# Optimization experiments

Measured on AMD Instinct MI355X. Metric: run time of the kernel, lower is better.

Reference implementation:

```python
import jax, jax.numpy as jnp
import numpy as np

N = 100000
E = 1600000
IN_C, HID_C, OUT_C = 128, 64, 32


def _add_self_loops(edge_index, n):
    loops = jnp.arange(n, dtype=edge_index.dtype)
    src = jnp.concatenate([edge_index[0], loops])
    dst = jnp.concatenate([edge_index[1], loops])
    return src, dst


def _gcn_norm(src, dst, n):
    # symmetric normalization on A + I with unit edge weights
    deg = jax.ops.segment_sum(jnp.ones_like(dst, dtype=jnp.float32), dst, num_segments=n)
    dinv = jnp.where(deg > 0, jax.lax.rsqrt(deg), 0.0)
    return dinv[src] * dinv[dst]  # [E+N]


def _gcn_conv(x, src, dst, norm, W, b, n):
    h = x @ W                              # [N, out]
    msg = h[src] * norm[:, None]           # [E+N, out]  (dominant gather)
    out = jax.ops.segment_sum(msg, dst, num_segments=n)
    return out + b


def setup_inputs() -> dict:
    key = jax.random.key(0)
    k = jax.random.split(key, 6)
    x = jax.random.normal(k[0], (N, IN_C), dtype=jnp.float32)
    edge_index = jax.random.randint(k[1], (2, E), 0, N, dtype=jnp.int32)
    # Glorot-style init for GCN weights
    W1 = jax.random.normal(k[2], (IN_C, HID_C), dtype=jnp.float32) / np.sqrt(IN_C)
    b1 = jnp.zeros((HID_C,), dtype=jnp.float32)
    W2 = jax.random.normal(k[3], (HID_C, OUT_C), dtype=jnp.float32) / np.sqrt(HID_C)
    b2 = jnp.zeros((OUT_C,), dtype=jnp.float32)
    return {"x": x, "edge_index": edge_index, "W1": W1, "b1": b1, "W2": W2, "b2": b2}


def reference(x, edge_index, W1, b1, W2, b2):
    src, dst = _add_self_loops(edge_index, N)
    norm = _gcn_norm(src, dst, N)
    h = _gcn_conv(x, src, dst, norm, W1, b1, N)
    h = jax.nn.relu(h)
    # dropout p=0.2 is identity in eval mode
    out = _gcn_conv(h, src, dst, norm, W2, b2, N)
    return out
```

## Files before the change

kernel.cpp:

```cpp
#include <hip/hip_runtime.h>
#include <hip/hip_fp16.h>

#define N_NODES 100000
#define E_EDGES 1600000
#define IN_C 128
#define HID_C 64
#define OUT_C 32
#define BNODES 64
#define NBUCK ((N_NODES + BNODES - 1) / BNODES)
#define MAXB 2048
#define NCHUNK 256
#define CHUNK_E (E_EDGES / NCHUNK)

__device__ __forceinline__ int chunk_of_block(int b) { return (b & 7) * (NCHUNK / 8) + (b >> 3); }

__global__ void zero_gcur_kernel(int* __restrict__ gcur) {
    int i = blockIdx.x * 256 + threadIdx.x;
    if (i < NBUCK) gcur[i] = 0;
}

__global__ __launch_bounds__(1024) void bucket_scatter_kernel(const int* __restrict__ src,
                                                              const int* __restrict__ dst,
                                                              int* __restrict__ gcur,
                                                              unsigned* __restrict__ pairs) {
    __shared__ int h[NBUCK];
    for (int i = threadIdx.x; i < NBUCK; i += 1024) h[i] = 0;
    __syncthreads();
    const int chunk = chunk_of_block(blockIdx.x);
    const int base = chunk * CHUNK_E;
    int dc[7];
    int nj = 0;
    for (int j = threadIdx.x; j < CHUNK_E; j += 1024) {
        int d = dst[base + j];
        dc[nj++] = d;
        atomicAdd(&h[d >> 6], 1);
    }
    __syncthreads();
    for (int i = threadIdx.x; i < NBUCK; i += 1024) {
        int c = h[i];
        if (c > 0) h[i] = atomicAdd(&gcur[i], c);
    }
    __syncthreads();
    nj = 0;
    for (int j = threadIdx.x; j < CHUNK_E; j += 1024) {
        int d = dc[nj++];
        int pos = atomicAdd(&h[d >> 6], 1);
        pairs[(unsigned)(d >> 6) * MAXB + (unsigned)pos] =
            ((unsigned)src[base + j] << 6) | (unsigned)(d & 63);
    }
}

__global__ __launch_bounds__(256) void bucket_sort_kernel(const int* __restrict__ gcur,
                                                          unsigned* __restrict__ pairs,
                                                          int* __restrict__ row_beg,
                                                          int* __restrict__ row_end,
                                                          float* __restrict__ dinv) {
    __shared__ unsigned sp[MAXB];
    __shared__ int hcnt[BNODES], scn[BNODES], cur[BNODES];
    const int b = blockIdx.x;
    const int beg = b * MAXB;
    int cnt = gcur[b];
    if (cnt > MAXB) cnt = MAXB;
    if (threadIdx.x < BNODES) hcnt[threadIdx.x] = 0;
    __syncthreads();
    for (int j = threadIdx.x; j < cnt; j += 256) {
        unsigned p = pairs[beg + j];
        sp[j] = p;
        atomicAdd(&hcnt[p & 63], 1);
    }
    __syncthreads();
    if (threadIdx.x < BNODES) scn[threadIdx.x] = hcnt[threadIdx.x];
    __syncthreads();
    for (int off = 1; off < BNODES; off <<= 1) {
        int t = 0;
        if (threadIdx.x < BNODES && threadIdx.x >= off) t = scn[threadIdx.x - off];
        __syncthreads();
        if (threadIdx.x < BNODES) scn[threadIdx.x] += t;
        __syncthreads();
    }
    if (threadIdx.x < BNODES) {
        int ex = scn[threadIdx.x] - hcnt[threadIdx.x];
        cur[threadIdx.x] = ex;
        int node = b * BNODES + threadIdx.x;
        if (node < N_NODES) {
            row_beg[node] = beg + ex;
            row_end[node] = beg + ex + hcnt[threadIdx.x];
            dinv[node] = rsqrtf((float)hcnt[threadIdx.x] + 1.0f);
        }
    }
    __syncthreads();
    for (int j = threadIdx.x; j < cnt; j += 256) {
        unsigned p = sp[j];
        int pos = atomicAdd(&cur[p & 63], 1);
        pairs[beg + pos] = p >> 6;
    }
}

__global__ __launch_bounds__(256) void gemm1_kernel(const float* __restrict__ x,
                                                    const float* __restrict__ W1,
                                                    const float* __restrict__ dinv,
                                                    __half* __restrict__ hs) {
    __shared__ float sW[IN_C * HID_C];
    for (int i = threadIdx.x; i < IN_C * HID_C; i += 256) sW[i] = W1[i];
    __syncthreads();
    const int cg = (threadIdx.x & 7) * 8;
    const int row0 = blockIdx.x * 64 + (threadIdx.x >> 3) * 2;
    float acc[2][8];
#pragma unroll
    for (int r = 0; r < 2; ++r)
#pragma unroll
        for (int c = 0; c < 8; ++c) acc[r][c] = 0.f;

    int rr[2];
#pragma unroll
    for (int r = 0; r < 2; ++r) rr[r] = min(row0 + r, N_NODES - 1);

    const float4* x4 = (const float4*)x;
#pragma unroll 2
    for (int k4 = 0; k4 < IN_C / 4; ++k4) {
        float4 xv[2];
#pragma unroll
        for (int r = 0; r < 2; ++r) xv[r] = x4[(size_t)rr[r] * (IN_C / 4) + k4];
        float xs[2][4];
#pragma unroll
        for (int r = 0; r < 2; ++r) {
            xs[r][0] = xv[r].x; xs[r][1] = xv[r].y; xs[r][2] = xv[r].z; xs[r][3] = xv[r].w;
        }
#pragma unroll
        for (int kk = 0; kk < 4; ++kk) {
            const float4* wp = (const float4*)(sW + (k4 * 4 + kk) * HID_C + cg);
            float4 w0 = wp[0], w1 = wp[1];
            float wv[8] = {w0.x, w0.y, w0.z, w0.w, w1.x, w1.y, w1.z, w1.w};
#pragma unroll
            for (int r = 0; r < 2; ++r)
#pragma unroll
                for (int c = 0; c < 8; ++c)
                    acc[r][c] = fmaf(xs[r][kk], wv[c], acc[r][c]);
        }
    }
#pragma unroll
    for (int r = 0; r < 2; ++r) {
        int row = row0 + r;
        if (row < N_NODES) {
            float dv = dinv[row];
            union { float4 f; __half2 h[4]; } u;
#pragma unroll
            for (int q = 0; q < 4; ++q)
                u.h[q] = __floats2half2_rn(acc[r][2 * q] * dv, acc[r][2 * q + 1] * dv);
            *(float4*)(hs + (size_t)row * HID_C + cg) = u.f;
        }
    }
}

__global__ __launch_bounds__(256) void agg1_kernel(const int* __restrict__ row_beg,
                                                   const int* __restrict__ row_end,
                                                   const int* __restrict__ col,
                                                   const float2* __restrict__ hsf,
                                                   const float* __restrict__ dinv,
                                                   const float* __restrict__ b1,
                                                   const float* __restrict__ W2,
                                                   __half* __restrict__ gs) {
    __shared__ float sW[HID_C * OUT_C];
    __shared__ __half2 sh2[16][HID_C / 2];
    for (int i = threadIdx.x; i < HID_C * OUT_C; i += 256) sW[i] = W2[i];

    const int nl = threadIdx.x >> 4;
    const int node = blockIdx.x * 16 + nl;
    const int lane = threadIdx.x & 15;
    const int beg = row_beg[node], end = row_end[node];
    float2 u = hsf[(size_t)node * 16 + lane];
    __half2* uh = (__half2*)&u;
    float2 t0 = __half22float2(uh[0]), t1 = __half22float2(uh[1]);
    float a0 = t0.x, a1 = t0.y, a2 = t1.x, a3 = t1.y;

    int j = beg;
    int idx0 = j + (lane & 7);
    int cv = (idx0 < end) ? col[idx0] : 0;
    while (j + 8 <= end) {
        int jn = j + 8;
        int idxn = jn + (lane & 7);
        int cvn = (idxn < end) ? col[idxn] : 0;
        int s[8];
#pragma unroll
        for (int e = 0; e < 8; ++e) s[e] = __shfl(cv, e, 8);
        float2 v[8];
#pragma unroll
        for (int e = 0; e < 8; ++e) v[e] = hsf[(size_t)s[e] * 16 + lane];
        cv = cvn;
#pragma unroll
        for (int e = 0; e < 8; ++e) {
            __half2* vh = (__half2*)&v[e];
            float2 w0 = __half22float2(vh[0]), w1 = __half22float2(vh[1]);
            a0 += w0.x; a1 += w0.y; a2 += w1.x; a3 += w1.y;
        }
        j = jn;
    }
    const int tail = end - j;
    for (int e = 0; e < tail; ++e) {
        int s = __shfl(cv, e, 8);
        float2 v = hsf[(size_t)s * 16 + lane];
        __half2* vh = (__half2*)&v;
        float2 w0 = __half22float2(vh[0]), w1 = __half22float2(vh[1]);
        a0 += w0.x; a1 += w0.y; a2 += w1.x; a3 += w1.y;
    }
    const float dv = dinv[node];
    float4 bb = ((const float4*)b1)[lane];
    __half2 p0 = __floats2half2_rn(fmaxf(dv * a0 + bb.x, 0.f), fmaxf(dv * a1 + bb.y, 0.f));
    __half2 p1 = __floats2half2_rn(fmaxf(dv * a2 + bb.z, 0.f), fmaxf(dv * a3 + bb.w, 0.f));
    sh2[nl][lane * 2] = p0;
    sh2[nl][lane * 2 + 1] = p1;
    __syncthreads();

    const int oc = lane * 2;
    float o0 = 0.f, o1 = 0.f;
#pragma unroll
    for (int k2 = 0; k2 < HID_C / 2; ++k2) {
        float2 hv = __half22float2(sh2[nl][k2]);
        const float* w0 = sW + (2 * k2) * OUT_C + oc;
        const float* w1 = sW + (2 * k2 + 1) * OUT_C + oc;
        o0 = fmaf(hv.x, w0[0], o0); o1 = fmaf(hv.x, w0[1], o1);
        o0 = fmaf(hv.y, w1[0], o0); o1 = fmaf(hv.y, w1[1], o1);
    }
    *(__half2*)(gs + (size_t)node * OUT_C + oc) = __floats2half2_rn(o0 * dv, o1 * dv);
}

__global__ void agg2_kernel(const int* __restrict__ row_beg, const int* __restrict__ row_end,
                            const int* __restrict__ col,
                            const float2* __restrict__ gsf, const float* __restrict__ dinv,
                            const float* __restrict__ b2, float* __restrict__ out) {
    const int node = blockIdx.x * 32 + (threadIdx.x >> 3);
    const int lane = threadIdx.x & 7;
    if (node >= N_NODES) return;
    const int beg = row_beg[node], end = row_end[node];
    float2 u = gsf[(size_t)node * 8 + lane];
    __half2* uh = (__half2*)&u;
    float2 t0 = __half22float2(uh[0]), t1 = __half22float2(uh[1]);
    float a0 = t0.x, a1 = t0.y, a2 = t1.x, a3 = t1.y;

    int j = beg;
    int idx0 = j + lane;
    int cv = (idx0 < end) ? col[idx0] : 0;
    while (j + 8 <= end) {
        int jn = j + 8;
        int idxn = jn + lane;
        int cvn = (idxn < end) ? col[idxn] : 0;
        int s[8];
#pragma unroll
        for (int e = 0; e < 8; ++e) s[e] = __shfl(cv, e, 8);
        float2 v[8];
#pragma unroll
        for (int e = 0; e < 8; ++e) v[e] = gsf[(size_t)s[e] * 8 + lane];
        cv = cvn;
#pragma unroll
        for (int e = 0; e < 8; ++e) {
            __half2* vh = (__half2*)&v[e];
            float2 w0 = __half22float2(vh[0]), w1 = __half22float2(vh[1]);
            a0 += w0.x; a1 += w0.y; a2 += w1.x; a3 += w1.y;
        }
        j = jn;
    }
    const int tail = end - j;
    for (int e = 0; e < tail; ++e) {
        int s = __shfl(cv, e, 8);
        float2 v = gsf[(size_t)s * 8 + lane];
        __half2* vh = (__half2*)&v;
        float2 w0 = __half22float2(vh[0]), w1 = __half22float2(vh[1]);
        a0 += w0.x; a1 += w0.y; a2 += w1.x; a3 += w1.y;
    }
    float dv = dinv[node];
    float4 bb = ((const float4*)b2)[lane];
    float4 o;
    o.x = dv * a0 + bb.x;
    o.y = dv * a1 + bb.y;
    o.z = dv * a2 + bb.z;
    o.w = dv * a3 + bb.w;
    *(float4*)(out + (size_t)node * OUT_C + lane * 4) = o;
}

extern "C" void kernel_launch(void* const* d_in, const int* in_sizes, int n_in,
                              void* d_out, int out_size, void* d_ws, size_t ws_size,
                              hipStream_t stream) {
    const float* x  = (const float*)d_in[0];
    const int*   ei = (const int*)d_in[1];
    const float* W1 = (const float*)d_in[2];
    const float* b1 = (const float*)d_in[3];
    const float* W2 = (const float*)d_in[4];
    const float* b2 = (const float*)d_in[5];
    float* out = (float*)d_out;

    const int* srcv = ei;
    const int* dstv = ei + E_EDGES;

    float* dinv  = (float*)d_ws;
    __half* hs   = (__half*)(dinv + N_NODES);
    __half* gs   = hs + (size_t)N_NODES * HID_C;
    int* row_beg = (int*)(gs + (size_t)N_NODES * OUT_C);
    int* row_end = row_beg + N_NODES;
    int* gcur    = row_end + N_NODES;
    unsigned* pairs = (unsigned*)(gcur + 1568);
    int* col = (int*)pairs;

    zero_gcur_kernel<<<(NBUCK + 255) / 256, 256, 0, stream>>>(gcur);
    bucket_scatter_kernel<<<NCHUNK, 1024, 0, stream>>>(srcv, dstv, gcur, pairs);
    bucket_sort_kernel<<<NBUCK, 256, 0, stream>>>(gcur, pairs, row_beg, row_end, dinv);

    gemm1_kernel<<<(N_NODES + 63) / 64, 256, 0, stream>>>(x, W1, dinv, hs);

    agg1_kernel<<<N_NODES / 16, 256, 0, stream>>>(row_beg, row_end, col,
                                                  (const float2*)hs, dinv, b1, W2, gs);

    agg2_kernel<<<(N_NODES + 31) / 32, 256, 0, stream>>>(row_beg, row_end, col,
                                                         (const float2*)gs, dinv, b2, out);
}
```

Baseline: 126.8 us.

## Double-buffer neighbor gathers in aggregation kernels with prefetched tail chunk

Restructures both aggregation kernels so two 8-edge chunks of neighbor features are gathered ahead while the previous chunk is consumed, and the partial tail chunk is issued up front. More gathers are in flight per thread, which targets the latency of the random gathers. Index math also switches from 64-bit to 32-bit unsigned, and the shared-memory reads in the fused W2 projection are padded and vectorized. The cost is higher register pressure from three 8-element buffers, and the removed bounds check in agg2 assumes the grid exactly covers all nodes.

```diff
diff --git a/kernel.cpp b/kernel.cpp
--- a/kernel.cpp
+++ b/kernel.cpp
@@ -152,6 +152,20 @@
     }
 }
 
+#define AG_GATHER(V, CV, TBL, STRIDE)                                         \
+    _Pragma("unroll")                                                         \
+    for (int e = 0; e < 8; ++e) {                                             \
+        int s_ = __shfl((CV), e, 8);                                          \
+        (V)[e] = (TBL)[(unsigned)(s_ * (STRIDE) + lane)];                     \
+    }
+#define AG_CONSUME(V)                                                         \
+    _Pragma("unroll")                                                         \
+    for (int e = 0; e < 8; ++e) {                                             \
+        __half2* vh_ = (__half2*)&(V)[e];                                     \
+        float2 w0_ = __half22float2(vh_[0]), w1_ = __half22float2(vh_[1]);    \
+        a0 += w0_.x; a1 += w0_.y; a2 += w1_.x; a3 += w1_.y;                   \
+    }
+
 __global__ __launch_bounds__(256) void agg1_kernel(const int* __restrict__ row_beg,
                                                    const int* __restrict__ row_end,
                                                    const int* __restrict__ col,
@@ -161,48 +175,57 @@
                                                    const float* __restrict__ W2,
                                                    __half* __restrict__ gs) {
     __shared__ float sW[HID_C * OUT_C];
-    __shared__ __half2 sh2[16][HID_C / 2];
+    __shared__ __half2 sh2[16][HID_C / 2 + 1];
     for (int i = threadIdx.x; i < HID_C * OUT_C; i += 256) sW[i] = W2[i];
 
     const int nl = threadIdx.x >> 4;
     const int node = blockIdx.x * 16 + nl;
     const int lane = threadIdx.x & 15;
     const int beg = row_beg[node], end = row_end[node];
-    float2 u = hsf[(size_t)node * 16 + lane];
+    const int deg = end - beg;
+    const int F = deg >> 3;
+
+    float2 u = hsf[(unsigned)(node * 16 + lane)];
     __half2* uh = (__half2*)&u;
     float2 t0 = __half22float2(uh[0]), t1 = __half22float2(uh[1]);
     float a0 = t0.x, a1 = t0.y, a2 = t1.x, a3 = t1.y;
 
-    int j = beg;
-    int idx0 = j + (lane & 7);
-    int cv = (idx0 < end) ? col[idx0] : 0;
-    while (j + 8 <= end) {
-        int jn = j + 8;
-        int idxn = jn + (lane & 7);
-        int cvn = (idxn < end) ? col[idxn] : 0;
-        int s[8];
-#pragma unroll
-        for (int e = 0; e < 8; ++e) s[e] = __shfl(cv, e, 8);
-        float2 v[8];
-#pragma unroll
-        for (int e = 0; e < 8; ++e) v[e] = hsf[(size_t)s[e] * 16 + lane];
-        cv = cvn;
-#pragma unroll
-        for (int e = 0; e < 8; ++e) {
-            __half2* vh = (__half2*)&v[e];
+    float2 vA[8], vB[8], vT[8];
+    int cvA = 0, cvB = 0, cvT = 0;
+    if (F >= 1) { cvA = col[beg + (lane & 7)];     AG_GATHER(vA, cvA, hsf, 16); }
+    if (F >= 2) { cvB = col[beg + 8 + (lane & 7)]; AG_GATHER(vB, cvB, hsf, 16); }
+    {
+        int ti = beg + F * 8 + (lane & 7);
+        cvT = (ti < end) ? col[ti] : 0;
+        AG_GATHER(vT, cvT, hsf, 16);
+    }
+    int c = 0;
+    while (c + 2 < F) {
+        int cvN = col[beg + (c + 2) * 8 + (lane & 7)];
+        AG_CONSUME(vA);
+        AG_GATHER(vA, cvN, hsf, 16);
+        ++c;
+        if (c + 2 < F) {
+            int cvN2 = col[beg + (c + 2) * 8 + (lane & 7)];
+            AG_CONSUME(vB);
+            AG_GATHER(vB, cvN2, hsf, 16);
+            ++c;
+        }
+    }
+    while (c < F) {
+        if ((c & 1) == 0) { AG_CONSUME(vA); } else { AG_CONSUME(vB); }
+        ++c;
+    }
+    const int tail = deg & 7;
+#pragma unroll
+    for (int e = 0; e < 8; ++e) {
+        if (e < tail) {
+            __half2* vh = (__half2*)&vT[e];
             float2 w0 = __half22float2(vh[0]), w1 = __half22float2(vh[1]);
             a0 += w0.x; a1 += w0.y; a2 += w1.x; a3 += w1.y;
         }
-        j = jn;
-    }
-    const int tail = end - j;
-    for (int e = 0; e < tail; ++e) {
-        int s = __shfl(cv, e, 8);
-        float2 v = hsf[(size_t)s * 16 + lane];
-        __half2* vh = (__half2*)&v;
-        float2 w0 = __half22float2(vh[0]), w1 = __half22float2(vh[1]);
-        a0 += w0.x; a1 += w0.y; a2 += w1.x; a3 += w1.y;
-    }
+    }
+
     const float dv = dinv[node];
     float4 bb = ((const float4*)b1)[lane];
     __half2 p0 = __floats2half2_rn(fmaxf(dv * a0 + bb.x, 0.f), fmaxf(dv * a1 + bb.y, 0.f));
@@ -212,16 +235,17 @@
     __syncthreads();
 
     const int oc = lane * 2;
+    const float2* wp2 = (const float2*)sW;
     float o0 = 0.f, o1 = 0.f;
 #pragma unroll
     for (int k2 = 0; k2 < HID_C / 2; ++k2) {
         float2 hv = __half22float2(sh2[nl][k2]);
-        const float* w0 = sW + (2 * k2) * OUT_C + oc;
-        const float* w1 = sW + (2 * k2 + 1) * OUT_C + oc;
-        o0 = fmaf(hv.x, w0[0], o0); o1 = fmaf(hv.x, w0[1], o1);
-        o0 = fmaf(hv.y, w1[0], o0); o1 = fmaf(hv.y, w1[1], o1);
-    }
-    *(__half2*)(gs + (size_t)node * OUT_C + oc) = __floats2half2_rn(o0 * dv, o1 * dv);
+        float2 wa = wp2[(2 * k2) * (OUT_C / 2) + (oc >> 1)];
+        float2 wb = wp2[(2 * k2 + 1) * (OUT_C / 2) + (oc >> 1)];
+        o0 = fmaf(hv.x, wa.x, o0); o1 = fmaf(hv.x, wa.y, o1);
+        o0 = fmaf(hv.y, wb.x, o0); o1 = fmaf(hv.y, wb.y, o1);
+    }
+    *(__half2*)(gs + (unsigned)(node * OUT_C + oc)) = __floats2half2_rn(o0 * dv, o1 * dv);
 }
 
 __global__ void agg2_kernel(const int* __restrict__ row_beg, const int* __restrict__ row_end,
@@ -230,42 +254,49 @@
                             const float* __restrict__ b2, float* __restrict__ out) {
     const int node = blockIdx.x * 32 + (threadIdx.x >> 3);
     const int lane = threadIdx.x & 7;
-    if (node >= N_NODES) return;
     const int beg = row_beg[node], end = row_end[node];
-    float2 u = gsf[(size_t)node * 8 + lane];
+    const int deg = end - beg;
+    const int F = deg >> 3;
+
+    float2 u = gsf[(unsigned)(node * 8 + lane)];
     __half2* uh = (__half2*)&u;
     float2 t0 = __half22float2(uh[0]), t1 = __half22float2(uh[1]);
     float a0 = t0.x, a1 = t0.y, a2 = t1.x, a3 = t1.y;
 
-    int j = beg;
-    int idx0 = j + lane;
-    int cv = (idx0 < end) ? col[idx0] : 0;
-    while (j + 8 <= end) {
-        int jn = j + 8;
-        int idxn = jn + lane;
-        int cvn = (idxn < end) ? col[idxn] : 0;
-        int s[8];
-#pragma unroll
-        for (int e = 0; e < 8; ++e) s[e] = __shfl(cv, e, 8);
-        float2 v[8];
-#pragma unroll
-        for (int e = 0; e < 8; ++e) v[e] = gsf[(size_t)s[e] * 8 + lane];
-        cv = cvn;
-#pragma unroll
-        for (int e = 0; e < 8; ++e) {
-            __half2* vh = (__half2*)&v[e];
+    float2 vA[8], vB[8], vT[8];
+    int cvA = 0, cvB = 0, cvT = 0;
+    if (F >= 1) { cvA = col[beg + lane];     AG_GATHER(vA, cvA, gsf, 8); }
+    if (F >= 2) { cvB = col[beg + 8 + lane]; AG_GATHER(vB, cvB, gsf, 8); }
+    {
+        int ti = beg + F * 8 + lane;
+        cvT = (ti < end) ? col[ti] : 0;
+        AG_GATHER(vT, cvT, gsf, 8);
+    }
+    int c = 0;
+    while (c + 2 < F) {
+        int cvN = col[beg + (c + 2) * 8 + lane];
+        AG_CONSUME(vA);
+        AG_GATHER(vA, cvN, gsf, 8);
+        ++c;
+        if (c + 2 < F) {
+            int cvN2 = col[beg + (c + 2) * 8 + lane];
+            AG_CONSUME(vB);
+            AG_GATHER(vB, cvN2, gsf, 8);
+            ++c;
+        }
+    }
+    while (c < F) {
+        if ((c & 1) == 0) { AG_CONSUME(vA); } else { AG_CONSUME(vB); }
+        ++c;
+    }
+    const int tail = deg & 7;
+#pragma unroll
+    for (int e = 0; e < 8; ++e) {
+        if (e < tail) {
+            __half2* vh = (__half2*)&vT[e];
             float2 w0 = __half22float2(vh[0]), w1 = __half22float2(vh[1]);
             a0 += w0.x; a1 += w0.y; a2 += w1.x; a3 += w1.y;
         }
-        j = jn;
-    }
-    const int tail = end - j;
-    for (int e = 0; e < tail; ++e) {
-        int s = __shfl(cv, e, 8);
-        float2 v = gsf[(size_t)s * 8 + lane];
-        __half2* vh = (__half2*)&v;
-        float2 w0 = __half22float2(vh[0]), w1 = __half22float2(vh[1]);
-        a0 += w0.x; a1 += w0.y; a2 += w1.x; a3 += w1.y;
     }
     float dv = dinv[node];
     float4 bb = ((const float4*)b2)[lane];
@@ -274,7 +305,7 @@
     o.y = dv * a1 + bb.y;
     o.z = dv * a2 + bb.z;
     o.w = dv * a3 + bb.w;
-    *(float4*)(out + (size_t)node * OUT_C + lane * 4) = o;
+    *(float4*)(out + (unsigned)(node * OUT_C + lane * 4)) = o;
 }
 
 extern "C" void kernel_launch(void* const* d_in, const int* in_sizes, int n_in,
```

Measured after the change: 133.4 us. +5.2%, slower.

## Replace bucket sort CSR build with fixed-capacity per-node adjacency slots

Applied to the files above, without the earlier changes.

Removes the two-pass bucket scatter and sort, and instead scatters each edge directly into a 64-slot per-node array using a global atomic counter per destination node. The counters double as degrees, so dinv is recomputed inline with rsqrt rather than stored. This cuts kernel launches and the sort pass. The risks are global atomic contention, a larger padded column array, and silently dropping edges for nodes with more than 64 in-edges.

```diff
diff --git a/kernel.cpp b/kernel.cpp
--- a/kernel.cpp
+++ b/kernel.cpp
@@ -6,99 +6,27 @@
 #define IN_C 128
 #define HID_C 64
 #define OUT_C 32
-#define BNODES 64
-#define NBUCK ((N_NODES + BNODES - 1) / BNODES)
-#define MAXB 2048
-#define NCHUNK 256
-#define CHUNK_E (E_EDGES / NCHUNK)
-
-__device__ __forceinline__ int chunk_of_block(int b) { return (b & 7) * (NCHUNK / 8) + (b >> 3); }
-
-__global__ void zero_gcur_kernel(int* __restrict__ gcur) {
+#define CAP 64
+
+__global__ void zero_ncur_kernel(int* __restrict__ ncur) {
     int i = blockIdx.x * 256 + threadIdx.x;
-    if (i < NBUCK) gcur[i] = 0;
-}
-
-__global__ __launch_bounds__(1024) void bucket_scatter_kernel(const int* __restrict__ src,
-                                                              const int* __restrict__ dst,
-                                                              int* __restrict__ gcur,
-                                                              unsigned* __restrict__ pairs) {
-    __shared__ int h[NBUCK];
-    for (int i = threadIdx.x; i < NBUCK; i += 1024) h[i] = 0;
-    __syncthreads();
-    const int chunk = chunk_of_block(blockIdx.x);
-    const int base = chunk * CHUNK_E;
-    int dc[7];
-    int nj = 0;
-    for (int j = threadIdx.x; j < CHUNK_E; j += 1024) {
-        int d = dst[base + j];
-        dc[nj++] = d;
-        atomicAdd(&h[d >> 6], 1);
-    }
-    __syncthreads();
-    for (int i = threadIdx.x; i < NBUCK; i += 1024) {
-        int c = h[i];
-        if (c > 0) h[i] = atomicAdd(&gcur[i], c);
-    }
-    __syncthreads();
-    nj = 0;
-    for (int j = threadIdx.x; j < CHUNK_E; j += 1024) {
-        int d = dc[nj++];
-        int pos = atomicAdd(&h[d >> 6], 1);
-        pairs[(unsigned)(d >> 6) * MAXB + (unsigned)pos] =
-            ((unsigned)src[base + j] << 6) | (unsigned)(d & 63);
-    }
-}
-
-__global__ __launch_bounds__(256) void bucket_sort_kernel(const int* __restrict__ gcur,
-                                                          unsigned* __restrict__ pairs,
-                                                          int* __restrict__ row_beg,
-                                                          int* __restrict__ row_end,
-                                                          float* __restrict__ dinv) {
-    __shared__ unsigned sp[MAXB];
-    __shared__ int hcnt[BNODES], scn[BNODES], cur[BNODES];
-    const int b = blockIdx.x;
-    const int beg = b * MAXB;
-    int cnt = gcur[b];
-    if (cnt > MAXB) cnt = MAXB;
-    if (threadIdx.x < BNODES) hcnt[threadIdx.x] = 0;
-    __syncthreads();
-    for (int j = threadIdx.x; j < cnt; j += 256) {
-        unsigned p = pairs[beg + j];
-        sp[j] = p;
-        atomicAdd(&hcnt[p & 63], 1);
-    }
-    __syncthreads();
-    if (threadIdx.x < BNODES) scn[threadIdx.x] = hcnt[threadIdx.x];
-    __syncthreads();
-    for (int off = 1; off < BNODES; off <<= 1) {
-        int t = 0;
-        if (threadIdx.x < BNODES && threadIdx.x >= off) t = scn[threadIdx.x - off];
-        __syncthreads();
-        if (threadIdx.x < BNODES) scn[threadIdx.x] += t;
-        __syncthreads();
-    }
-    if (threadIdx.x < BNODES) {
-        int ex = scn[threadIdx.x] - hcnt[threadIdx.x];
-        cur[threadIdx.x] = ex;
-        int node = b * BNODES + threadIdx.x;
-        if (node < N_NODES) {
-            row_beg[node] = beg + ex;
-            row_end[node] = beg + ex + hcnt[threadIdx.x];
-            dinv[node] = rsqrtf((float)hcnt[threadIdx.x] + 1.0f);
-        }
-    }
-    __syncthreads();
-    for (int j = threadIdx.x; j < cnt; j += 256) {
-        unsigned p = sp[j];
-        int pos = atomicAdd(&cur[p & 63], 1);
-        pairs[beg + pos] = p >> 6;
-    }
+    if (i < N_NODES) ncur[i] = 0;
+}
+
+__global__ __launch_bounds__(256) void edge_scatter_kernel(const int* __restrict__ src,
+                                                           const int* __restrict__ dst,
+                                                           int* __restrict__ ncur,
+                                                           int* __restrict__ colp) {
+    int i = blockIdx.x * 256 + threadIdx.x;
+    int d = dst[i];
+    int s = src[i];
+    int pos = atomicAdd(&ncur[d], 1);
+    if (pos < CAP) colp[(d << 6) + pos] = s;
 }
 
 __global__ __launch_bounds__(256) void gemm1_kernel(const float* __restrict__ x,
                                                     const float* __restrict__ W1,
-                                                    const float* __restrict__ dinv,
+                                                    const int* __restrict__ ncur,
                                                     __half* __restrict__ hs) {
     __shared__ float sW[IN_C * HID_C];
     for (int i = threadIdx.x; i < IN_C * HID_C; i += 256) sW[i] = W1[i];
@@ -142,7 +70,7 @@
     for (int r = 0; r < 2; ++r) {
         int row = row0 + r;
         if (row < N_NODES) {
-            float dv = dinv[row];
+            float dv = rsqrtf((float)ncur[row] + 1.0f);
             union { float4 f; __half2 h[4]; } u;
 #pragma unroll
             for (int q = 0; q < 4; ++q)
@@ -152,11 +80,9 @@
     }
 }
 
-__global__ __launch_bounds__(256) void agg1_kernel(const int* __restrict__ row_beg,
-                                                   const int* __restrict__ row_end,
+__global__ __launch_bounds__(256) void agg1_kernel(const int* __restrict__ ncur,
                                                    const int* __restrict__ col,
                                                    const float2* __restrict__ hsf,
-                                                   const float* __restrict__ dinv,
                                                    const float* __restrict__ b1,
                                                    const float* __restrict__ W2,
                                                    __half* __restrict__ gs) {
@@ -167,7 +93,9 @@
     const int nl = threadIdx.x >> 4;
     const int node = blockIdx.x * 16 + nl;
     const int lane = threadIdx.x & 15;
-    const int beg = row_beg[node], end = row_end[node];
+    const int cnt = min(ncur[node], CAP);
+    const int beg = node << 6;
+    const int end = beg + cnt;
     float2 u = hsf[(size_t)node * 16 + lane];
     __half2* uh = (__half2*)&u;
     float2 t0 = __half22float2(uh[0]), t1 = __half22float2(uh[1]);
@@ -203,7 +131,7 @@
         float2 w0 = __half22float2(vh[0]), w1 = __half22float2(vh[1]);
         a0 += w0.x; a1 += w0.y; a2 += w1.x; a3 += w1.y;
     }
-    const float dv = dinv[node];
+    const float dv = rsqrtf((float)cnt + 1.0f);
     float4 bb = ((const float4*)b1)[lane];
     __half2 p0 = __floats2half2_rn(fmaxf(dv * a0 + bb.x, 0.f), fmaxf(dv * a1 + bb.y, 0.f));
     __half2 p1 = __floats2half2_rn(fmaxf(dv * a2 + bb.z, 0.f), fmaxf(dv * a3 + bb.w, 0.f));
@@ -224,14 +152,15 @@
     *(__half2*)(gs + (size_t)node * OUT_C + oc) = __floats2half2_rn(o0 * dv, o1 * dv);
 }
 
-__global__ void agg2_kernel(const int* __restrict__ row_beg, const int* __restrict__ row_end,
+__global__ void agg2_kernel(const int* __restrict__ ncur,
                             const int* __restrict__ col,
-                            const float2* __restrict__ gsf, const float* __restrict__ dinv,
+                            const float2* __restrict__ gsf,
                             const float* __restrict__ b2, float* __restrict__ out) {
     const int node = blockIdx.x * 32 + (threadIdx.x >> 3);
     const int lane = threadIdx.x & 7;
-    if (node >= N_NODES) return;
-    const int beg = row_beg[node], end = row_end[node];
+    const int cnt = min(ncur[node], CAP);
+    const int beg = node << 6;
+    const int end = beg + cnt;
     float2 u = gsf[(size_t)node * 8 + lane];
     __half2* uh = (__half2*)&u;
     float2 t0 = __half22float2(uh[0]), t1 = __half22float2(uh[1]);
@@ -267,7 +196,7 @@
         float2 w0 = __half22float2(vh[0]), w1 = __half22float2(vh[1]);
         a0 += w0.x; a1 += w0.y; a2 += w1.x; a3 += w1.y;
     }
-    float dv = dinv[node];
+    float dv = rsqrtf((float)cnt + 1.0f);
     float4 bb = ((const float4*)b2)[lane];
     float4 o;
     o.x = dv * a0 + bb.x;
@@ -291,24 +220,19 @@
     const int* srcv = ei;
     const int* dstv = ei + E_EDGES;
 
-    float* dinv  = (float*)d_ws;
-    __half* hs   = (__half*)(dinv + N_NODES);
+    __half* hs   = (__half*)d_ws;
     __half* gs   = hs + (size_t)N_NODES * HID_C;
-    int* row_beg = (int*)(gs + (size_t)N_NODES * OUT_C);
-    int* row_end = row_beg + N_NODES;
-    int* gcur    = row_end + N_NODES;
-    unsigned* pairs = (unsigned*)(gcur + 1568);
-    int* col = (int*)pairs;
-
-    zero_gcur_kernel<<<(NBUCK + 255) / 256, 256, 0, stream>>>(gcur);
-    bucket_scatter_kernel<<<NCHUNK, 1024, 0, stream>>>(srcv, dstv, gcur, pairs);
-    bucket_sort_kernel<<<NBUCK, 256, 0, stream>>>(gcur, pairs, row_beg, row_end, dinv);
-
-    gemm1_kernel<<<(N_NODES + 63) / 64, 256, 0, stream>>>(x, W1, dinv, hs);
-
-    agg1_kernel<<<N_NODES / 16, 256, 0, stream>>>(row_beg, row_end, col,
-                                                  (const float2*)hs, dinv, b1, W2, gs);
-
-    agg2_kernel<<<(N_NODES + 31) / 32, 256, 0, stream>>>(row_beg, row_end, col,
-                                                         (const float2*)gs, dinv, b2, out);
-}
+    int* ncur    = (int*)(gs + (size_t)N_NODES * OUT_C);
+    int* colp    = ncur + N_NODES;
+
+    zero_ncur_kernel<<<(N_NODES + 255) / 256, 256, 0, stream>>>(ncur);
+    edge_scatter_kernel<<<E_EDGES / 256, 256, 0, stream>>>(srcv, dstv, ncur, colp);
+
+    gemm1_kernel<<<(N_NODES + 63) / 64, 256, 0, stream>>>(x, W1, ncur, hs);
+
+    agg1_kernel<<<N_NODES / 16, 256, 0, stream>>>(ncur, colp, (const float2*)hs,
+                                                  b1, W2, gs);
+
+    agg2_kernel<<<(N_NODES + 31) / 32, 256, 0, stream>>>(ncur, colp, (const float2*)gs,
+                                                         b2, out);
+}
```

New measurement: 216.6 us. +70.8%, slower.
